# Performance work log

Hardware: AMD Instinct MI355X
Metric: run time of the kernel (lower is better)

## Reference

```python
import jax, jax.numpy as jnp
import numpy as np

N, E, D = 50000, 300000, 64
ETYPES = ['temporal', 'assigned_to', 'com', 'tin', 'win', 'sin', 'take_time', 'use_time']


def setup_inputs():
    key = jax.random.key(0)
    ks = iter(jax.random.split(key, 80))

    def nrm(shape, s=1.0):
        return jax.random.normal(next(ks), shape, dtype=jnp.float32) * s

    inp = {}
    inp['feat_task'] = nrm((N, D))
    inp['feat_worker'] = nrm((N, D))
    inp['feat_state'] = nrm((N, D))
    for et in ETYPES:
        inp['src_' + et] = jax.random.randint(next(ks), (E,), 0, N, dtype=jnp.int32)
        inp['dst_' + et] = jax.random.randint(next(ks), (E,), 0, N, dtype=jnp.int32)
    inp['w_temporal'] = jax.random.uniform(next(ks), (E, 1), dtype=jnp.float32)
    inp['t_take_time'] = jax.random.uniform(next(ks), (E, 1), dtype=jnp.float32)
    inp['t_use_time'] = jax.random.uniform(next(ks), (E, 1), dtype=jnp.float32)
    for et in ETYPES:
        inp['W_' + et] = nrm((D, D), 0.05)
        inp['b_' + et] = nrm((D,), 0.05)
    for nm in ['edge_fc', 'edge_fc_ttr', 'edge_fc_rut']:
        inp[nm + '_W'] = nrm((D, 1), 0.05)
        inp[nm + '_b'] = nrm((D,), 0.05)
    inp['attn_W'] = nrm((1, 3 * D), 0.05)
    inp['attn_ttr_W'] = nrm((1, 3 * D), 0.05)
    inp['attn_rut_W'] = nrm((1, 3 * D), 0.05)
    inp['attn_assigned_W'] = nrm((1, 2 * D), 0.05)
    inp['attn_com_W'] = nrm((1, 2 * D), 0.05)
    inp['attn_tin_W'] = nrm((1, 2 * D), 0.05)
    inp['attn_rin_W'] = nrm((1, 2 * D), 0.05)
    return inp


def _seg_softmax_sum(e, msg, dst, n):
    # numerically stable segment softmax over each dst node's incoming edges,
    # followed by the alpha-weighted scatter-sum (DGL reduce_func).
    m = jax.ops.segment_max(e, dst, num_segments=n)        # [n,1]
    ex = jnp.exp(e - m[dst])                               # [E,1]
    den = jax.ops.segment_sum(ex, dst, num_segments=n)     # [n,1]
    return jax.ops.segment_sum((ex / den[dst]) * msg, dst, num_segments=n)


def _gat(Wh_s, Wh_d, src, dst, aW, n, zij=None):
    # e = leaky_relu(attn_fc(concat(z_src, z_dst[, zij]))); the concat is never
    # materialized -- attn weight is split into per-block dot products.
    d = Wh_s.shape[1]
    zs = Wh_s[src]
    e = zs @ aW[0, :d] + Wh_d[dst] @ aW[0, d:2 * d]
    if zij is not None:
        e = e + zij @ aW[0, 2 * d:]
        msg = zs + zij   # message_func: src Wh + edge embedding
    else:
        msg = zs
    e = jax.nn.leaky_relu(e, 0.2)[:, None]
    return _seg_softmax_sum(e, msg, dst, n)


def _forward(feat_task, feat_worker, feat_state, w_temporal, t_take_time, t_use_time,
             W_temporal, b_temporal, W_assigned_to, b_assigned_to, W_com, b_com,
             W_tin, b_tin, W_win, b_win, W_sin, b_sin, W_take_time, b_take_time,
             W_use_time, b_use_time, edge_fc_W, edge_fc_b, edge_fc_ttr_W, edge_fc_ttr_b,
             edge_fc_rut_W, edge_fc_rut_b, attn_W, attn_assigned_W, attn_com_W,
             attn_tin_W, attn_rin_W, attn_ttr_W, attn_rut_W,
             src_temporal, dst_temporal, src_assigned_to, dst_assigned_to,
             src_com, dst_com, src_tin, dst_tin, src_win, dst_win,
             src_sin, dst_sin, src_take_time, dst_take_time, src_use_time, dst_use_time):
    n_task, n_worker, n_state = feat_task.shape[0], feat_worker.shape[0], feat_state.shape[0]
    # Equation (1): per-etype linear projection of source node features
    Wh_temporal = feat_task @ W_temporal.T + b_temporal
    Wh_assigned = feat_task @ W_assigned_to.T + b_assigned_to
    Wh_com = feat_worker @ W_com.T + b_com
    Wh_tin = feat_task @ W_tin.T + b_tin
    Wh_win = feat_worker @ W_win.T + b_win
    Wh_sin = feat_state @ W_sin.T + b_sin
    Wh_ttr = feat_task @ W_take_time.T + b_take_time
    Wh_rut = feat_worker @ W_use_time.T + b_use_time
    # per-edge scalar feature -> d-dim embedding
    zij_t = w_temporal @ edge_fc_W.T + edge_fc_b
    zij_ttr = t_take_time @ edge_fc_ttr_W.T + edge_fc_ttr_b
    zij_rut = t_use_time @ edge_fc_rut_W.T + edge_fc_rut_b
    # Equations (2)-(4): per-etype attention + segment softmax + scatter-sum
    h_temporal = _gat(Wh_temporal, Wh_temporal, src_temporal, dst_temporal, attn_W, n_task, zij_t)
    h_assigned = _gat(Wh_assigned, Wh_com, src_assigned_to, dst_assigned_to, attn_assigned_W, n_worker)
    h_com = _gat(Wh_com, Wh_com, src_com, dst_com, attn_com_W, n_worker)
    h_tin = _gat(Wh_tin, Wh_sin, src_tin, dst_tin, attn_tin_W, n_state)
    h_win = _gat(Wh_win, Wh_sin, src_win, dst_win, attn_rin_W, n_state)
    h_sin = jax.ops.segment_sum(Wh_sin[src_sin], dst_sin, num_segments=n_state)  # copy_src + sum
    h_ttr = _gat(Wh_ttr, Wh_com, src_take_time, dst_take_time, attn_ttr_W, n_worker, zij_ttr)
    h_rut = _gat(Wh_rut, Wh_temporal, src_use_time, dst_use_time, attn_rut_W, n_task, zij_rut)
    # multi_update_all cross-type 'sum', then ReLU
    h_task = jax.nn.relu(h_temporal + h_rut)
    h_worker = jax.nn.relu(h_assigned + h_com + h_ttr)
    h_state = jax.nn.relu(h_tin + h_win + h_sin)
    return jnp.stack([h_task, h_worker, h_state])  # [3, N, D]


def reference(feat_task, feat_worker, feat_state,
              src_temporal, dst_temporal, src_assigned_to, dst_assigned_to,
              src_com, dst_com, src_tin, dst_tin, src_win, dst_win,
              src_sin, dst_sin, src_take_time, dst_take_time, src_use_time, dst_use_time,
              w_temporal, t_take_time, t_use_time,
              W_temporal, b_temporal, W_assigned_to, b_assigned_to, W_com, b_com,
              W_tin, b_tin, W_win, b_win, W_sin, b_sin, W_take_time, b_take_time,
              W_use_time, b_use_time, edge_fc_W, edge_fc_b, edge_fc_ttr_W, edge_fc_ttr_b,
              edge_fc_rut_W, edge_fc_rut_b, attn_W, attn_ttr_W, attn_rut_W,
              attn_assigned_W, attn_com_W, attn_tin_W, attn_rin_W):
    return _forward(feat_task, feat_worker, feat_state, w_temporal, t_take_time, t_use_time,
                    W_temporal, b_temporal, W_assigned_to, b_assigned_to, W_com, b_com,
                    W_tin, b_tin, W_win, b_win, W_sin, b_sin, W_take_time, b_take_time,
                    W_use_time, b_use_time, edge_fc_W, edge_fc_b, edge_fc_ttr_W, edge_fc_ttr_b,
                    edge_fc_rut_W, edge_fc_rut_b, attn_W, attn_assigned_W, attn_com_W,
                    attn_tin_W, attn_rin_W, attn_ttr_W, attn_rut_W,
                    src_temporal, dst_temporal, src_assigned_to, dst_assigned_to,
                    src_com, dst_com, src_tin, dst_tin, src_win, dst_win,
                    src_sin, dst_sin, src_take_time, dst_take_time, src_use_time, dst_use_time)
```

## Files before the change

### kernel.cpp

```cpp
#include <hip/hip_runtime.h>
#include <math.h>

#define NN 50000
#define EE 300000
#define NG 8
#define NTOT (NG * NN)
#define NTOT9 (9 * NN)
#define NBKT 782
#define BCAP 3584
#define TILE 1024
#define NBLKE ((EE + TILE - 1) / TILE)

typedef unsigned short u16;
typedef unsigned int u32;
typedef short bf16x8 __attribute__((ext_vector_type(8)));
typedef float f32x16 __attribute__((ext_vector_type(16)));

__device__ __forceinline__ float b2f(u16 u) { return __uint_as_float(((u32)u) << 16); }
__device__ __forceinline__ u16 f2b(float f) {
    u32 x = __float_as_uint(f);
    u32 lsb = (x >> 16) & 1u;
    return (u16)((x + 0x7fffu + lsb) >> 16);
}

__global__ void HeteroGATLayer_14259291423309_kernel() {}

__global__ void k_zeroi(int* p, int n) {
    int i = blockIdx.x * 256 + threadIdx.x;
    if (i < n) p[i] = 0;
}

struct ProjP { const float* feat[8]; const float* W[8]; const float* b[8]; u16* wh[8]; };

__global__ __launch_bounds__(256) void k_proj(ProjP p) {
    __shared__ u16 sA[64 * 64];
    __shared__ u16 sB[64 * 64];
    const int t = blockIdx.y;
    const int tid = threadIdx.x;
    const int row0 = blockIdx.x * 64;
    const float* feat = p.feat[t];
    const float* W = p.W[t];

    #pragma unroll
    for (int q = 0; q < 4; ++q) {
        int idx = q * 256 + tid;
        int r = idx >> 4;
        int c4 = (idx & 15) * 4;
        int gr = row0 + r;
        if (gr >= NN) gr = NN - 1;
        float4 fv = *(const float4*)(feat + (size_t)gr * 64 + c4);
        *(ushort4*)&sA[r * 64 + c4] = make_ushort4(f2b(fv.x), f2b(fv.y), f2b(fv.z), f2b(fv.w));
        float4 wv = *(const float4*)(W + (size_t)r * 64 + c4);
        *(ushort4*)&sB[r * 64 + c4] = make_ushort4(f2b(wv.x), f2b(wv.y), f2b(wv.z), f2b(wv.w));
    }
    __syncthreads();

    const int wv = tid >> 6, lane = tid & 63;
    const int mrow = (wv & 1) * 32, ncol = (wv >> 1) * 32;
    const int half = lane >> 5, l31 = lane & 31;

    f32x16 acc;
    #pragma unroll
    for (int i = 0; i < 16; ++i) acc[i] = 0.0f;

    #pragma unroll
    for (int k0 = 0; k0 < 64; k0 += 16) {
        bf16x8 af = *(const bf16x8*)&sA[(mrow + l31) * 64 + k0 + half * 8];
        bf16x8 bf = *(const bf16x8*)&sB[(ncol + l31) * 64 + k0 + half * 8];
        acc = __builtin_amdgcn_mfma_f32_32x32x16_bf16(af, bf, acc, 0, 0, 0);
    }

    float bb = p.b[t][ncol + l31];
    u16* whp = p.wh[t];
    #pragma unroll
    for (int reg = 0; reg < 16; ++reg) {
        int rowD = (reg & 3) + 8 * (reg >> 2) + 4 * half;
        int gr = row0 + mrow + rowD;
        if (gr < NN) whp[(size_t)gr * 64 + ncol + l31] = f2b(acc[reg] + bb);
    }
}

struct NdP { const u16* whs[7]; const u16* whd[7]; const float* attn[7]; float* el; float* er; };

__global__ __launch_bounds__(256) void k_nodedot(NdP p) {
    const int g = blockIdx.y;
    const int tid = threadIdx.x;
    const int node = blockIdx.x * 16 + (tid >> 4);
    const int l16 = tid & 15;
    ushort4 a = *(const ushort4*)(p.whs[g] + (size_t)node * 64 + l16 * 4);
    ushort4 b = *(const ushort4*)(p.whd[g] + (size_t)node * 64 + l16 * 4);
    float4 wa = *(const float4*)(p.attn[g] + l16 * 4);
    float4 wb = *(const float4*)(p.attn[g] + 64 + l16 * 4);
    float x = b2f(a.x) * wa.x + b2f(a.y) * wa.y + b2f(a.z) * wa.z + b2f(a.w) * wa.w;
    float y = b2f(b.x) * wb.x + b2f(b.y) * wb.y + b2f(b.z) * wb.z + b2f(b.w) * wb.w;
    #pragma unroll
    for (int off = 8; off; off >>= 1) {
        x += __shfl_xor(x, off);
        y += __shfl_xor(y, off);
    }
    if (l16 == 0) {
        p.el[g * NN + node] = x;
        p.er[g * NN + node] = y;
    }
}

struct ZP { const float* attn[3]; const float* fcW[3]; const float* fcb[3]; float* c[3]; };

__global__ void k_zconst(ZP p) {
    int z = blockIdx.x;
    if (threadIdx.x != 0) return;
    float c1 = 0.f, c0 = 0.f;
    for (int k = 0; k < 64; ++k) {
        float a2 = p.attn[z][128 + k];
        c1 += p.fcW[z][k] * a2;
        c0 += p.fcb[z][k] * a2;
    }
    p.c[z][0] = c1;
    p.c[z][1] = c0;
}

struct BinAP {
    const int* src[8]; const int* dst[8]; const float* w[8];
    const float* el[8]; const float* er[8];
    const float* consts;
    int whoff[8];
    int* gcur; int4* bkt;
};

__global__ __launch_bounds__(256) void k_binA(BinAP p) {
    __shared__ int hist[128];
    const int g = blockIdx.y;
    const int b0 = (g * NN) >> 9;
    const int tid = threadIdx.x;
    const int e = blockIdx.x * TILE + tid * 4;
    if (tid < 128) hist[tid] = 0;

    const bool hw = p.w[g] != 0;
    float c1 = 0.f, c0 = 0.f;
    if (g < 7 && hw) { c1 = p.consts[2 * g]; c0 = p.consts[2 * g + 1]; }
    const int wo = p.whoff[g];

    int sr[4], bl[4], low[4];
    float sc[4], pw[4];
    const bool valid = e < EE;
    if (valid) {
        int4 s4 = *(const int4*)(p.src[g] + e);
        int4 d4 = *(const int4*)(p.dst[g] + e);
        float4 w4 = make_float4(0.f, 0.f, 0.f, 0.f);
        if (hw) w4 = *(const float4*)(p.w[g] + e);
        int ss[4] = {s4.x, s4.y, s4.z, s4.w};
        int dd[4] = {d4.x, d4.y, d4.z, d4.w};
        float ww[4] = {w4.x, w4.y, w4.z, w4.w};
        #pragma unroll
        for (int q = 0; q < 4; ++q) {
            int key = g * NN + dd[q];
            bl[q] = (key >> 9) - b0;
            low[q] = key & 511;
            sr[q] = wo + (ss[q] << 7);
            float scv = 1.0f, pwv = 0.0f;
            if (g < 7) {
                scv = p.el[g][ss[q]] + p.er[g][dd[q]];
                if (hw) scv += c1 * ww[q] + c0;
                scv = scv > 0.f ? scv : 0.2f * scv;
                scv = __expf(scv);
                if (hw) pwv = scv * ww[q];
            }
            sc[q] = scv; pw[q] = pwv;
        }
    }
    __syncthreads();
    if (valid) {
        #pragma unroll
        for (int q = 0; q < 4; ++q) atomicAdd(&hist[bl[q]], 1);
    }
    __syncthreads();
    if (tid < 128) {
        int c = hist[tid];
        hist[tid] = c ? atomicAdd(&p.gcur[b0 + tid], c) : 0;
    }
    __syncthreads();
    if (valid) {
        #pragma unroll
        for (int q = 0; q < 4; ++q) {
            int pos = atomicAdd(&hist[bl[q]], 1);
            int4 v;
            v.x = sr[q];
            v.y = __float_as_int(sc[q]);
            v.z = __float_as_int(pw[q]);
            v.w = low[q];
            p.bkt[(size_t)(b0 + bl[q]) * BCAP + pos] = v;
        }
    }
}

__global__ __launch_bounds__(512) void k_binB(const int* __restrict__ gcur,
                                              const int4* __restrict__ bkt,
                                              int2* __restrict__ csr,
                                              int4* __restrict__ rowdeg) {
    __shared__ int2 st2[BCAP];
    __shared__ float st3[BCAP];
    __shared__ int hist[512];
    __shared__ int scn[512];
    __shared__ int wsum[8];
    const int b = blockIdx.x;
    const int tid = threadIdx.x;
    int count = gcur[b];
    if (count > BCAP) count = BCAP;
    hist[tid] = 0;
    __syncthreads();
    const int4* src = bkt + (size_t)b * BCAP;
    for (int i = tid; i < count; i += 512) atomicAdd(&hist[src[i].w], 1);
    __syncthreads();
    int h = hist[tid];
    const int lane = tid & 63, wvi = tid >> 6;
    int incl = h;
    #pragma unroll
    for (int off = 1; off < 64; off <<= 1) {
        int t = __shfl_up(incl, off);
        if (lane >= off) incl += t;
    }
    if (lane == 63) wsum[wvi] = incl;
    __syncthreads();
    int wb = 0;
    #pragma unroll
    for (int w = 0; w < 8; ++w)
        if (w < wvi) wb += wsum[w];
    const int excl = wb + incl - h;
    scn[tid] = excl;
    __syncthreads();
    for (int i = tid; i < count; i += 512) {
        int4 v = src[i];
        int pos = atomicAdd(&scn[v.w], 1);
        st2[pos] = make_int2(v.x, v.y);
        st3[pos] = __int_as_float(v.z);
    }
    __syncthreads();
    float den = 0.f, sw = 0.f;
    for (int j = 0; j < h; ++j) {
        den += __int_as_float(st2[excl + j].y);
        sw += st3[excl + j];
    }
    const int gkey = b * 512 + tid;
    if (gkey < NTOT) {
        float inv = (gkey >= 7 * NN) ? 1.0f : ((h > 0 && den > 0.f) ? 1.0f / den : 0.f);
        u32 beg = (u32)(b * BCAP + excl);
        rowdeg[gkey] = make_int4((int)((beg << 10) | (u32)h),
                                 __float_as_int(inv), __float_as_int(sw * inv), 0);
    }
    for (int i = tid; i < count; i += 512) csr[(size_t)b * BCAP + i] = st2[i];
}

struct GathP {
    int gidx[3][3]; int hasfc[3][3];
    const float* fcW[3][3]; const float* fcb[3][3];
    const int4* rowdeg; const int2* csr;
    const char* whArena;
    float* out;
};

__device__ __forceinline__ void chunk_acc(const char* whA, int dby, int2 v, int len,
                                          float& vs0, float& vs1) {
    int myS = v.x;
    float mySc = __int_as_float(v.y);
    int k = 0;
    for (; k + 4 <= len; k += 4) {
        int s0 = __shfl(myS, k), s1 = __shfl(myS, k + 1);
        int s2 = __shfl(myS, k + 2), s3 = __shfl(myS, k + 3);
        float a0 = __shfl(mySc, k), a1 = __shfl(mySc, k + 1);
        float a2 = __shfl(mySc, k + 2), a3 = __shfl(mySc, k + 3);
        vs0 += a0 * b2f(*(const u16*)(whA + (u32)(s0 + dby)));
        vs1 += a1 * b2f(*(const u16*)(whA + (u32)(s1 + dby)));
        vs0 += a2 * b2f(*(const u16*)(whA + (u32)(s2 + dby)));
        vs1 += a3 * b2f(*(const u16*)(whA + (u32)(s3 + dby)));
    }
    for (; k < len; ++k) {
        int s = __shfl(myS, k);
        float a = __shfl(mySc, k);
        vs0 += a * b2f(*(const u16*)(whA + (u32)(s + dby)));
    }
}

__global__ __launch_bounds__(256) void k_gather(GathP p) {
    const int tg = blockIdx.y;
    const int wv = threadIdx.x >> 6, d = threadIdx.x & 63;
    const int i = blockIdx.x * 4 + wv;
    if (i >= NN) return;
    const int dby = 2 * d;
    const char* whA = p.whArena;

    int4 rd[3];
    #pragma unroll
    for (int t = 0; t < 3; ++t) rd[t] = p.rowdeg[p.gidx[tg][t] * NN + i];
    int2 sv[3];
    #pragma unroll
    for (int t = 0; t < 3; ++t) {
        int dg = rd[t].x & 1023;
        u32 beg = ((u32)rd[t].x) >> 10;
        sv[t] = (d < dg) ? p.csr[beg + d] : make_int2(0, 0);
    }

    float tot = 0.f;
    #pragma unroll
    for (int t = 0; t < 3; ++t) {
        int dg = rd[t].x & 1023;
        if (dg == 0) continue;
        u32 beg = ((u32)rd[t].x) >> 10;
        float vs0 = 0.f, vs1 = 0.f;
        int len0 = dg < 64 ? dg : 64;
        chunk_acc(whA, dby, sv[t], len0, vs0, vs1);
        for (u32 base = beg + 64; base < beg + (u32)dg; base += 64) {
            int len = (int)(beg + (u32)dg - base);
            if (len > 64) len = 64;
            int2 v = (d < len) ? p.csr[base + d] : make_int2(0, 0);
            chunk_acc(whA, dby, v, len, vs0, vs1);
        }
        tot += (vs0 + vs1) * __int_as_float(rd[t].y);
        if (p.hasfc[tg][t])
            tot += p.fcW[tg][t][d] * __int_as_float(rd[t].z) + p.fcb[tg][t][d];
    }
    p.out[((size_t)tg * NN + i) * 64 + d] = tot > 0.f ? tot : 0.f;
}

extern "C" void kernel_launch(void* const* d_in, const int* in_sizes, int n_in,
                              void* d_out, int out_size, void* d_ws, size_t ws_size,
                              hipStream_t stream) {
    (void)in_sizes; (void)n_in; (void)out_size; (void)ws_size;
    const float* feats[3] = {(const float*)d_in[0], (const float*)d_in[1], (const float*)d_in[2]};
    const int* srcs[8];
    const int* dsts[8];
    for (int t = 0; t < 8; ++t) {
        srcs[t] = (const int*)d_in[3 + 2 * t];
        dsts[t] = (const int*)d_in[4 + 2 * t];
    }
    const float* ew0 = (const float*)d_in[19];
    const float* ew1 = (const float*)d_in[20];
    const float* ew2 = (const float*)d_in[21];
    const float* Wm[8];
    const float* bm[8];
    for (int t = 0; t < 8; ++t) {
        Wm[t] = (const float*)d_in[22 + 2 * t];
        bm[t] = (const float*)d_in[23 + 2 * t];
    }
    const float* fcW0 = (const float*)d_in[38];
    const float* fcb0 = (const float*)d_in[39];
    const float* fcW1 = (const float*)d_in[40];
    const float* fcb1 = (const float*)d_in[41];
    const float* fcW2 = (const float*)d_in[42];
    const float* fcb2 = (const float*)d_in[43];
    const float* attn_W          = (const float*)d_in[44];
    const float* attn_ttr_W      = (const float*)d_in[45];
    const float* attn_rut_W      = (const float*)d_in[46];
    const float* attn_assigned_W = (const float*)d_in[47];
    const float* attn_com_W      = (const float*)d_in[48];
    const float* attn_tin_W      = (const float*)d_in[49];
    const float* attn_rin_W      = (const float*)d_in[50];

    u16* Wh = (u16*)d_ws;
    char* b0 = (char*)d_ws + (size_t)8 * NN * 64 * sizeof(u16);
    float* el     = (float*)b0;
    float* er     = el + (size_t)7 * NN;
    float* consts = er + (size_t)7 * NN;
    int* gcur     = (int*)(consts + 16);
    int4* rowdeg4 = (int4*)(((size_t)(gcur + NBKT) + 15) & ~(size_t)15);
    int4* bkt     = rowdeg4 + NTOT9;
    int2* csr     = (int2*)(bkt + (size_t)NBKT * BCAP);

    int g_et[8]   = {0, 1, 2, 3, 4, 6, 7, 5};
    int g_sidx[8] = {0, 1, 2, 3, 4, 6, 7, 5};
    int g_didx[7] = {0, 2, 2, 5, 5, 2, 0};
    const float* g_attn[7] = {attn_W, attn_assigned_W, attn_com_W, attn_tin_W,
                              attn_rin_W, attn_ttr_W, attn_rut_W};
    const float* g_w[8] = {ew0, 0, 0, 0, 0, ew1, ew2, 0};

    k_zeroi<<<(NBKT + 255) / 256, 256, 0, stream>>>(gcur, NBKT);
    k_zeroi<<<(4 * (NTOT9 - NTOT) + 255) / 256, 256, 0, stream>>>((int*)(rowdeg4 + NTOT),
                                                                  4 * (NTOT9 - NTOT));

    {
        ProjP pp;
        int fsel[8] = {0, 0, 1, 0, 1, 2, 0, 1};
        for (int t = 0; t < 8; ++t) {
            pp.feat[t] = feats[fsel[t]];
            pp.W[t] = Wm[t];
            pp.b[t] = bm[t];
            pp.wh[t] = Wh + (size_t)t * NN * 64;
        }
        k_proj<<<dim3(782, 8), 256, 0, stream>>>(pp);
    }

    {
        NdP np;
        for (int g = 0; g < 7; ++g) {
            np.whs[g] = Wh + (size_t)g_sidx[g] * NN * 64;
            np.whd[g] = Wh + (size_t)g_didx[g] * NN * 64;
            np.attn[g] = g_attn[g];
        }
        np.el = el; np.er = er;
        k_nodedot<<<dim3(NN / 16, 7), 256, 0, stream>>>(np);
    }
    {
        ZP zp;
        zp.attn[0] = attn_W;     zp.fcW[0] = fcW0; zp.fcb[0] = fcb0; zp.c[0] = consts + 0;
        zp.attn[1] = attn_ttr_W; zp.fcW[1] = fcW1; zp.fcb[1] = fcb1; zp.c[1] = consts + 10;
        zp.attn[2] = attn_rut_W; zp.fcW[2] = fcW2; zp.fcb[2] = fcb2; zp.c[2] = consts + 12;
        k_zconst<<<3, 64, 0, stream>>>(zp);
    }

    {
        BinAP bp;
        for (int g = 0; g < 8; ++g) {
            bp.src[g] = srcs[g_et[g]];
            bp.dst[g] = dsts[g_et[g]];
            bp.w[g] = g_w[g];
            bp.el[g] = (g < 7) ? el + (size_t)g * NN : 0;
            bp.er[g] = (g < 7) ? er + (size_t)g * NN : 0;
            bp.whoff[g] = g_sidx[g] * NN * 128;
        }
        bp.consts = consts;
        bp.gcur = gcur;
        bp.bkt = bkt;
        k_binA<<<dim3(NBLKE, 8), 256, 0, stream>>>(bp);
    }
    k_binB<<<NBKT, 512, 0, stream>>>(gcur, bkt, csr, rowdeg4);

    {
        GathP gp;
        gp.rowdeg = rowdeg4;
        gp.csr = csr;
        gp.whArena = (const char*)Wh;
        gp.out = (float*)d_out;
        gp.gidx[0][0] = 0; gp.hasfc[0][0] = 1; gp.fcW[0][0] = fcW0; gp.fcb[0][0] = fcb0;
        gp.gidx[0][1] = 6; gp.hasfc[0][1] = 1; gp.fcW[0][1] = fcW2; gp.fcb[0][1] = fcb2;
        gp.gidx[0][2] = 8; gp.hasfc[0][2] = 0; gp.fcW[0][2] = 0;    gp.fcb[0][2] = 0;
        gp.gidx[1][0] = 1; gp.hasfc[1][0] = 0; gp.fcW[1][0] = 0;    gp.fcb[1][0] = 0;
        gp.gidx[1][1] = 2; gp.hasfc[1][1] = 0; gp.fcW[1][1] = 0;    gp.fcb[1][1] = 0;
        gp.gidx[1][2] = 5; gp.hasfc[1][2] = 1; gp.fcW[1][2] = fcW1; gp.fcb[1][2] = fcb1;
        gp.gidx[2][0] = 3; gp.hasfc[2][0] = 0; gp.fcW[2][0] = 0;    gp.fcb[2][0] = 0;
        gp.gidx[2][1] = 4; gp.hasfc[2][1] = 0; gp.fcW[2][1] = 0;    gp.fcb[2][1] = 0;
        gp.gidx[2][2] = 7; gp.hasfc[2][2] = 0; gp.fcW[2][2] = 0;    gp.fcb[2][2] = 0;
        k_gather<<<dim3((NN + 3) / 4, 3), 256, 0, stream>>>(gp);
    }
}
```

Measured before the change: 395.8 us.

## Fuse attention node-dots into projection, share feature tiles, simplify gather loop

The projection kernel now loads each feature tile once and loops over every weight matrix that uses that feature. It writes the bf16 projection and also computes the attention dot products (el/er) from a shared-memory copy, so the separate node-dot kernel and its re-read of Wh go away. The gather kernel drops the shuffle-based chunked CSR walk. Instead it interleaves all three edge types per step, reading CSR entries through scalar readfirstlane loads, which raises memory-level parallelism but serializes the per-edge loads. The trade-off is fewer projection blocks, each doing more serial work, and a possible loss of ILP in the gather.

```diff
diff --git a/kernel.cpp b/kernel.cpp
--- a/kernel.cpp
+++ b/kernel.cpp
@@ -30,16 +30,24 @@
     if (i < n) p[i] = 0;
 }
 
-struct ProjP { const float* feat[8]; const float* W[8]; const float* b[8]; u16* wh[8]; };
+struct ProjP {
+    const float* feat[3];
+    const float* W[8]; const float* b[8];
+    u16* wh;
+    int ntile[3]; int tiles[3][4];
+    int nvec[8];
+    const float* avec[8][4];
+    float* dvec[8][4];
+};
 
 __global__ __launch_bounds__(256) void k_proj(ProjP p) {
     __shared__ u16 sA[64 * 64];
-    __shared__ u16 sB[64 * 64];
-    const int t = blockIdx.y;
+    __shared__ u16 sW[64 * 64];
+    __shared__ u16 sC[64 * 66];
+    const int f = blockIdx.y;
     const int tid = threadIdx.x;
     const int row0 = blockIdx.x * 64;
-    const float* feat = p.feat[t];
-    const float* W = p.W[t];
+    const float* feat = p.feat[f];
 
     #pragma unroll
     for (int q = 0; q < 4; ++q) {
@@ -50,57 +58,61 @@
         if (gr >= NN) gr = NN - 1;
         float4 fv = *(const float4*)(feat + (size_t)gr * 64 + c4);
         *(ushort4*)&sA[r * 64 + c4] = make_ushort4(f2b(fv.x), f2b(fv.y), f2b(fv.z), f2b(fv.w));
-        float4 wv = *(const float4*)(W + (size_t)r * 64 + c4);
-        *(ushort4*)&sB[r * 64 + c4] = make_ushort4(f2b(wv.x), f2b(wv.y), f2b(wv.z), f2b(wv.w));
-    }
-    __syncthreads();
+    }
 
     const int wv = tid >> 6, lane = tid & 63;
     const int mrow = (wv & 1) * 32, ncol = (wv >> 1) * 32;
     const int half = lane >> 5, l31 = lane & 31;
-
-    f32x16 acc;
-    #pragma unroll
-    for (int i = 0; i < 16; ++i) acc[i] = 0.0f;
-
-    #pragma unroll
-    for (int k0 = 0; k0 < 64; k0 += 16) {
-        bf16x8 af = *(const bf16x8*)&sA[(mrow + l31) * 64 + k0 + half * 8];
-        bf16x8 bf = *(const bf16x8*)&sB[(ncol + l31) * 64 + k0 + half * 8];
-        acc = __builtin_amdgcn_mfma_f32_32x32x16_bf16(af, bf, acc, 0, 0, 0);
-    }
-
-    float bb = p.b[t][ncol + l31];
-    u16* whp = p.wh[t];
-    #pragma unroll
-    for (int reg = 0; reg < 16; ++reg) {
-        int rowD = (reg & 3) + 8 * (reg >> 2) + 4 * half;
-        int gr = row0 + mrow + rowD;
-        if (gr < NN) whp[(size_t)gr * 64 + ncol + l31] = f2b(acc[reg] + bb);
-    }
-}
-
-struct NdP { const u16* whs[7]; const u16* whd[7]; const float* attn[7]; float* el; float* er; };
-
-__global__ __launch_bounds__(256) void k_nodedot(NdP p) {
-    const int g = blockIdx.y;
-    const int tid = threadIdx.x;
-    const int node = blockIdx.x * 16 + (tid >> 4);
-    const int l16 = tid & 15;
-    ushort4 a = *(const ushort4*)(p.whs[g] + (size_t)node * 64 + l16 * 4);
-    ushort4 b = *(const ushort4*)(p.whd[g] + (size_t)node * 64 + l16 * 4);
-    float4 wa = *(const float4*)(p.attn[g] + l16 * 4);
-    float4 wb = *(const float4*)(p.attn[g] + 64 + l16 * 4);
-    float x = b2f(a.x) * wa.x + b2f(a.y) * wa.y + b2f(a.z) * wa.z + b2f(a.w) * wa.w;
-    float y = b2f(b.x) * wb.x + b2f(b.y) * wb.y + b2f(b.z) * wb.z + b2f(b.w) * wb.w;
-    #pragma unroll
-    for (int off = 8; off; off >>= 1) {
-        x += __shfl_xor(x, off);
-        y += __shfl_xor(y, off);
-    }
-    if (l16 == 0) {
-        p.el[g * NN + node] = x;
-        p.er[g * NN + node] = y;
+    const int nt = p.ntile[f];
+
+    for (int ti = 0; ti < nt; ++ti) {
+        const int t = p.tiles[f][ti];
+        const float* W = p.W[t];
+        #pragma unroll
+        for (int q = 0; q < 4; ++q) {
+            int idx = q * 256 + tid;
+            int r = idx >> 4;
+            int c4 = (idx & 15) * 4;
+            float4 wv4 = *(const float4*)(W + r * 64 + c4);
+            *(ushort4*)&sW[r * 64 + c4] = make_ushort4(f2b(wv4.x), f2b(wv4.y), f2b(wv4.z), f2b(wv4.w));
+        }
+        __syncthreads();
+
+        f32x16 acc;
+        #pragma unroll
+        for (int i = 0; i < 16; ++i) acc[i] = 0.0f;
+        #pragma unroll
+        for (int k0 = 0; k0 < 64; k0 += 16) {
+            bf16x8 af = *(const bf16x8*)&sA[(mrow + l31) * 64 + k0 + half * 8];
+            bf16x8 bf = *(const bf16x8*)&sW[(ncol + l31) * 64 + k0 + half * 8];
+            acc = __builtin_amdgcn_mfma_f32_32x32x16_bf16(af, bf, acc, 0, 0, 0);
+        }
+
+        float bb = p.b[t][ncol + l31];
+        u16* whp = p.wh + (size_t)t * NN * 64;
+        #pragma unroll
+        for (int reg = 0; reg < 16; ++reg) {
+            int rowD = (reg & 3) + 8 * (reg >> 2) + 4 * half;
+            int gr = row0 + mrow + rowD;
+            u16 c16 = f2b(acc[reg] + bb);
+            if (gr < NN) whp[(size_t)gr * 64 + ncol + l31] = c16;
+            sC[(mrow + rowD) * 66 + ncol + l31] = c16;
+        }
+        __syncthreads();
+
+        const int r = tid & 63, j = tid >> 6;
+        if (j < p.nvec[t]) {
+            const float* av = p.avec[t][j];
+            float s = 0.f;
+            #pragma unroll
+            for (int c = 0; c < 64; c += 4) {
+                ushort4 cv = *(const ushort4*)&sC[r * 66 + c];
+                float4 a4 = *(const float4*)(av + c);
+                s += b2f(cv.x) * a4.x + b2f(cv.y) * a4.y + b2f(cv.z) * a4.z + b2f(cv.w) * a4.w;
+            }
+            int gr = row0 + r;
+            if (gr < NN) p.dvec[t][j][gr] = s;
+        }
     }
 }
 
@@ -253,72 +265,64 @@
 struct GathP {
     int gidx[3][3]; int hasfc[3][3];
     const float* fcW[3][3]; const float* fcb[3][3];
-    const int4* rowdeg; const int2* csr;
-    const char* whArena;
-    float* out;
 };
 
-__device__ __forceinline__ void chunk_acc(const char* whA, int dby, int2 v, int len,
-                                          float& vs0, float& vs1) {
-    int myS = v.x;
-    float mySc = __int_as_float(v.y);
-    int k = 0;
-    for (; k + 4 <= len; k += 4) {
-        int s0 = __shfl(myS, k), s1 = __shfl(myS, k + 1);
-        int s2 = __shfl(myS, k + 2), s3 = __shfl(myS, k + 3);
-        float a0 = __shfl(mySc, k), a1 = __shfl(mySc, k + 1);
-        float a2 = __shfl(mySc, k + 2), a3 = __shfl(mySc, k + 3);
-        vs0 += a0 * b2f(*(const u16*)(whA + (u32)(s0 + dby)));
-        vs1 += a1 * b2f(*(const u16*)(whA + (u32)(s1 + dby)));
-        vs0 += a2 * b2f(*(const u16*)(whA + (u32)(s2 + dby)));
-        vs1 += a3 * b2f(*(const u16*)(whA + (u32)(s3 + dby)));
-    }
-    for (; k < len; ++k) {
-        int s = __shfl(myS, k);
-        float a = __shfl(mySc, k);
-        vs0 += a * b2f(*(const u16*)(whA + (u32)(s + dby)));
-    }
-}
-
-__global__ __launch_bounds__(256) void k_gather(GathP p) {
+__global__ __launch_bounds__(256) void k_gather(GathP p,
+        const int4* __restrict__ rowdeg, const int2* __restrict__ csr,
+        const char* __restrict__ whA, float* __restrict__ out) {
     const int tg = blockIdx.y;
     const int wv = threadIdx.x >> 6, d = threadIdx.x & 63;
     const int i = blockIdx.x * 4 + wv;
-    if (i >= NN) return;
     const int dby = 2 * d;
-    const char* whA = p.whArena;
-
-    int4 rd[3];
-    #pragma unroll
-    for (int t = 0; t < 3; ++t) rd[t] = p.rowdeg[p.gidx[tg][t] * NN + i];
-    int2 sv[3];
+
+    int len[3]; u32 beg[3]; float inv[3], sw[3];
     #pragma unroll
     for (int t = 0; t < 3; ++t) {
-        int dg = rd[t].x & 1023;
-        u32 beg = ((u32)rd[t].x) >> 10;
-        sv[t] = (d < dg) ? p.csr[beg + d] : make_int2(0, 0);
+        int4 rv = rowdeg[p.gidx[tg][t] * NN + i];
+        int rx = __builtin_amdgcn_readfirstlane(rv.x);
+        len[t] = rx & 1023;
+        beg[t] = ((u32)rx) >> 10;
+        inv[t] = __uint_as_float((u32)__builtin_amdgcn_readfirstlane(rv.y));
+        sw[t] = __uint_as_float((u32)__builtin_amdgcn_readfirstlane(rv.z));
+    }
+    int kmax = len[0] > len[1] ? len[0] : len[1];
+    kmax = kmax > len[2] ? kmax : len[2];
+    const int2* s0 = csr + beg[0];
+    const int2* s1 = csr + beg[1];
+    const int2* s2 = csr + beg[2];
+
+    float acc[3] = {0.f, 0.f, 0.f};
+    #pragma unroll 2
+    for (int k = 0; k < kmax; ++k) {
+        if (k < len[0]) {
+            int2 v = s0[k];
+            u32 ro = (u32)__builtin_amdgcn_readfirstlane(v.x);
+            float al = __uint_as_float((u32)__builtin_amdgcn_readfirstlane(v.y));
+            acc[0] += al * b2f(*(const u16*)(whA + ro + dby));
+        }
+        if (k < len[1]) {
+            int2 v = s1[k];
+            u32 ro = (u32)__builtin_amdgcn_readfirstlane(v.x);
+            float al = __uint_as_float((u32)__builtin_amdgcn_readfirstlane(v.y));
+            acc[1] += al * b2f(*(const u16*)(whA + ro + dby));
+        }
+        if (k < len[2]) {
+            int2 v = s2[k];
+            u32 ro = (u32)__builtin_amdgcn_readfirstlane(v.x);
+            float al = __uint_as_float((u32)__builtin_amdgcn_readfirstlane(v.y));
+            acc[2] += al * b2f(*(const u16*)(whA + ro + dby));
+        }
     }
 
     float tot = 0.f;
     #pragma unroll
     for (int t = 0; t < 3; ++t) {
-        int dg = rd[t].x & 1023;
-        if (dg == 0) continue;
-        u32 beg = ((u32)rd[t].x) >> 10;
-        float vs0 = 0.f, vs1 = 0.f;
-        int len0 = dg < 64 ? dg : 64;
-        chunk_acc(whA, dby, sv[t], len0, vs0, vs1);
-        for (u32 base = beg + 64; base < beg + (u32)dg; base += 64) {
-            int len = (int)(beg + (u32)dg - base);
-            if (len > 64) len = 64;
-            int2 v = (d < len) ? p.csr[base + d] : make_int2(0, 0);
-            chunk_acc(whA, dby, v, len, vs0, vs1);
-        }
-        tot += (vs0 + vs1) * __int_as_float(rd[t].y);
+        if (len[t] == 0) continue;
+        tot += acc[t] * inv[t];
         if (p.hasfc[tg][t])
-            tot += p.fcW[tg][t][d] * __int_as_float(rd[t].z) + p.fcb[tg][t][d];
-    }
-    p.out[((size_t)tg * NN + i) * 64 + d] = tot > 0.f ? tot : 0.f;
+            tot += p.fcW[tg][t][d] * sw[t] + p.fcb[tg][t][d];
+    }
+    out[((size_t)tg * NN + i) * 64 + d] = tot > 0.f ? tot : 0.f;
 }
 
 extern "C" void kernel_launch(void* const* d_in, const int* in_sizes, int n_in,
@@ -367,9 +371,6 @@
 
     int g_et[8]   = {0, 1, 2, 3, 4, 6, 7, 5};
     int g_sidx[8] = {0, 1, 2, 3, 4, 6, 7, 5};
-    int g_didx[7] = {0, 2, 2, 5, 5, 2, 0};
-    const float* g_attn[7] = {attn_W, attn_assigned_W, attn_com_W, attn_tin_W,
-                              attn_rin_W, attn_ttr_W, attn_rut_W};
     const float* g_w[8] = {ew0, 0, 0, 0, 0, ew1, ew2, 0};
 
     k_zeroi<<<(NBKT + 255) / 256, 256, 0, stream>>>(gcur, NBKT);
@@ -378,26 +379,30 @@
 
     {
         ProjP pp;
-        int fsel[8] = {0, 0, 1, 0, 1, 2, 0, 1};
+        pp.feat[0] = feats[0]; pp.feat[1] = feats[1]; pp.feat[2] = feats[2];
+        for (int t = 0; t < 8; ++t) { pp.W[t] = Wm[t]; pp.b[t] = bm[t]; }
+        pp.wh = Wh;
+        pp.ntile[0] = 4; pp.tiles[0][0] = 0; pp.tiles[0][1] = 1; pp.tiles[0][2] = 3; pp.tiles[0][3] = 6;
+        pp.ntile[1] = 3; pp.tiles[1][0] = 2; pp.tiles[1][1] = 4; pp.tiles[1][2] = 7; pp.tiles[1][3] = 0;
+        pp.ntile[2] = 1; pp.tiles[2][0] = 5; pp.tiles[2][1] = 0; pp.tiles[2][2] = 0; pp.tiles[2][3] = 0;
         for (int t = 0; t < 8; ++t) {
-            pp.feat[t] = feats[fsel[t]];
-            pp.W[t] = Wm[t];
-            pp.b[t] = bm[t];
-            pp.wh[t] = Wh + (size_t)t * NN * 64;
-        }
-        k_proj<<<dim3(782, 8), 256, 0, stream>>>(pp);
-    }
-
-    {
-        NdP np;
-        for (int g = 0; g < 7; ++g) {
-            np.whs[g] = Wh + (size_t)g_sidx[g] * NN * 64;
-            np.whd[g] = Wh + (size_t)g_didx[g] * NN * 64;
-            np.attn[g] = g_attn[g];
-        }
-        np.el = el; np.er = er;
-        k_nodedot<<<dim3(NN / 16, 7), 256, 0, stream>>>(np);
-    }
+            pp.nvec[t] = 0;
+            for (int j = 0; j < 4; ++j) { pp.avec[t][j] = 0; pp.dvec[t][j] = 0; }
+        }
+        auto setv = [&](int t, int j, const float* a, float* dv) { pp.avec[t][j] = a; pp.dvec[t][j] = dv; };
+        pp.nvec[0] = 3; setv(0, 0, attn_W, el);           setv(0, 1, attn_W + 64, er);
+                        setv(0, 2, attn_rut_W + 64, er + 6 * NN);
+        pp.nvec[1] = 1; setv(1, 0, attn_assigned_W, el + 1 * NN);
+        pp.nvec[2] = 4; setv(2, 0, attn_com_W, el + 2 * NN); setv(2, 1, attn_assigned_W + 64, er + 1 * NN);
+                        setv(2, 2, attn_com_W + 64, er + 2 * NN); setv(2, 3, attn_ttr_W + 64, er + 5 * NN);
+        pp.nvec[3] = 1; setv(3, 0, attn_tin_W, el + 3 * NN);
+        pp.nvec[4] = 1; setv(4, 0, attn_rin_W, el + 4 * NN);
+        pp.nvec[5] = 2; setv(5, 0, attn_tin_W + 64, er + 3 * NN); setv(5, 1, attn_rin_W + 64, er + 4 * NN);
+        pp.nvec[6] = 1; setv(6, 0, attn_ttr_W, el + 5 * NN);
+        pp.nvec[7] = 1; setv(7, 0, attn_rut_W, el + 6 * NN);
+        k_proj<<<dim3(782, 3), 256, 0, stream>>>(pp);
+    }
+
     {
         ZP zp;
         zp.attn[0] = attn_W;     zp.fcW[0] = fcW0; zp.fcb[0] = fcb0; zp.c[0] = consts + 0;
@@ -425,10 +430,6 @@
 
     {
         GathP gp;
-        gp.rowdeg = rowdeg4;
-        gp.csr = csr;
-        gp.whArena = (const char*)Wh;
-        gp.out = (float*)d_out;
         gp.gidx[0][0] = 0; gp.hasfc[0][0] = 1; gp.fcW[0][0] = fcW0; gp.fcb[0][0] = fcb0;
         gp.gidx[0][1] = 6; gp.hasfc[0][1] = 1; gp.fcW[0][1] = fcW2; gp.fcb[0][1] = fcb2;
         gp.gidx[0][2] = 8; gp.hasfc[0][2] = 0; gp.fcW[0][2] = 0;    gp.fcb[0][2] = 0;
@@ -438,6 +439,7 @@
         gp.gidx[2][0] = 3; gp.hasfc[2][0] = 0; gp.fcW[2][0] = 0;    gp.fcb[2][0] = 0;
         gp.gidx[2][1] = 4; gp.hasfc[2][1] = 0; gp.fcW[2][1] = 0;    gp.fcb[2][1] = 0;
         gp.gidx[2][2] = 7; gp.hasfc[2][2] = 0; gp.fcW[2][2] = 0;    gp.fcb[2][2] = 0;
-        k_gather<<<dim3((NN + 3) / 4, 3), 256, 0, stream>>>(gp);
-    }
-}
+        k_gather<<<dim3(NN / 4, 3), 256, 0, stream>>>(gp, rowdeg4, csr,
+                                                      (const char*)Wh, (float*)d_out);
+    }
+}
```

Result: slower. 440.5 us (+11.3%).
